# Kernel optimization log

Hardware: AMD Instinct MI355X
Metric: run time of the kernel (lower is better)

Reference implementation:

```python
import math
import jax, jax.numpy as jnp
import numpy as np

B, S, D = 32, 2048, 128

def setup_inputs() -> dict:
    key = jax.random.key(0)
    kq, kk, kv, km = jax.random.split(key, 4)
    q = jax.random.normal(kq, (B, S, D), dtype=jnp.float32)
    k = jax.random.normal(kk, (B, S, D), dtype=jnp.float32)
    v = jax.random.normal(kv, (B, S, D), dtype=jnp.float32)
    mask = jax.random.uniform(km, (B, S, S), dtype=jnp.float32)
    return {"q": q, "k": k, "v": v, "mask": mask}

def reference(q, k, v, mask):
    # scaled_product = (q @ k^T) / sqrt(d), then MULTIPLICATIVE mask, softmax, @ v
    scale = 1.0 / math.sqrt(k.shape[-1])
    scores = jnp.einsum("bqd,bkd->bqk", q, k) * scale  # [B, Sq, Sk]
    scores = scores * mask
    weights = jax.nn.softmax(scores, axis=-1)
    return jnp.einsum("bqk,bkd->bqd", weights, v)
```

## Files before the change

### kernel.cpp

```cpp
#include <hip/hip_runtime.h>
#include <math.h>

#define BATCH 32
#define SEQ   2048
#define DH    128
#define QT    64
#define KT    64
#define KSTR  136
#define VSTR  72
#define PSTR  72
#define SCALE 0.08838834764831845f

typedef _Float16 f16;
typedef _Float16 f16x4 __attribute__((ext_vector_type(4)));
typedef _Float16 f16x8 __attribute__((ext_vector_type(8)));
typedef float    f32x4 __attribute__((ext_vector_type(4)));

__global__ __launch_bounds__(256, 3)
void ScaledDotProductAttention_46720654246409_kernel(
    const float* __restrict__ q, const float* __restrict__ k,
    const float* __restrict__ v, const float* __restrict__ mask,
    float* __restrict__ out)
{
    __shared__ f16 ks[KT * KSTR];
    __shared__ f16 vs[DH * VSTR];
    __shared__ f16 ps[4 * 16 * PSTR];

    const int tid  = threadIdx.x;
    const int wv   = tid >> 6;
    const int lane = tid & 63;
    const int quad = lane >> 4;
    const int l16  = lane & 15;
    const int srow = tid >> 5;
    const int scol = tid & 31;

    const int bidx = blockIdx.x;
    const int b    = bidx >> 5;
    const int q0   = (bidx & 31) * QT;

    const size_t qkvBase = (size_t)b * SEQ * DH;
    const size_t mBase   = (size_t)b * SEQ * SEQ;

    #pragma unroll
    for (int p = 0; p < 8; ++p) {
        int r = p * 8 + srow;
        f32x4 x = *(const f32x4*)&q[qkvBase + (size_t)(q0 + r) * DH + scol * 4];
        f16x4 h = { (f16)x.x, (f16)x.y, (f16)x.z, (f16)x.w };
        *(f16x4*)&ks[r * KSTR + scol * 4] = h;
    }
    __syncthreads();

    f16x8 aq[4];
    #pragma unroll
    for (int dc = 0; dc < 4; ++dc)
        aq[dc] = *(const f16x8*)&ks[(wv * 16 + l16) * KSTR + dc * 32 + quad * 8];
    __syncthreads();

    float m_run[4] = { -INFINITY, -INFINITY, -INFINITY, -INFINITY };
    float l_run[4] = { 0.f, 0.f, 0.f, 0.f };
    f32x4 o[8];
    #pragma unroll
    for (int f = 0; f < 8; ++f) o[f] = (f32x4){0.f, 0.f, 0.f, 0.f};

    for (int kt = 0; kt < SEQ / KT; ++kt) {
        const int k0 = kt * KT;

        float mk[4][4];
        #pragma unroll
        for (int f = 0; f < 4; ++f)
            #pragma unroll
            for (int r = 0; r < 4; ++r)
                mk[f][r] = mask[mBase + (size_t)(q0 + wv*16 + quad*4 + r) * SEQ
                                + k0 + f*16 + l16];

        #pragma unroll
        for (int p = 0; p < 8; ++p) {
            int r = p * 8 + srow;
            f32x4 x = *(const f32x4*)&k[qkvBase + (size_t)(k0 + r) * DH + scol * 4];
            f16x4 h = { (f16)x.x, (f16)x.y, (f16)x.z, (f16)x.w };
            *(f16x4*)&ks[r * KSTR + scol * 4] = h;
        }
        #pragma unroll
        for (int p = 0; p < 8; ++p) {
            int j = p * 8 + srow;
            const float* vr = &v[qkvBase + (size_t)(k0 + j) * DH];
            #pragma unroll
            for (int i = 0; i < 4; ++i)
                vs[(scol + 32*i) * VSTR + j] = (f16)vr[scol + 32*i];
        }
        __syncthreads();

        f32x4 sc[4];
        #pragma unroll
        for (int f = 0; f < 4; ++f) {
            sc[f] = (f32x4){0.f, 0.f, 0.f, 0.f};
            #pragma unroll
            for (int dc = 0; dc < 4; ++dc) {
                f16x8 bk = *(const f16x8*)&ks[(f*16 + l16) * KSTR + dc*32 + quad*8];
                sc[f] = __builtin_amdgcn_mfma_f32_16x16x32_f16(aq[dc], bk, sc[f], 0, 0, 0);
            }
        }

        float pj[4][4];
        float alpha[4];
        #pragma unroll
        for (int r = 0; r < 4; ++r) {
            float sf[4];
            #pragma unroll
            for (int f = 0; f < 4; ++f) sf[f] = sc[f][r] * SCALE * mk[f][r];
            float mx = fmaxf(fmaxf(sf[0], sf[1]), fmaxf(sf[2], sf[3]));
            #pragma unroll
            for (int off = 1; off < 16; off <<= 1)
                mx = fmaxf(mx, __shfl_xor(mx, off, 16));
            float mn = fmaxf(m_run[r], mx);
            float al = __expf(m_run[r] - mn);
            float sum = 0.f;
            #pragma unroll
            for (int f = 0; f < 4; ++f) { pj[f][r] = __expf(sf[f] - mn); sum += pj[f][r]; }
            #pragma unroll
            for (int off = 1; off < 16; off <<= 1)
                sum += __shfl_xor(sum, off, 16);
            m_run[r] = mn;
            l_run[r] = l_run[r] * al + sum;
            alpha[r] = al;
        }

        #pragma unroll
        for (int f = 0; f < 4; ++f)
            #pragma unroll
            for (int r = 0; r < 4; ++r)
                ps[(wv*16 + quad*4 + r) * PSTR + f*16 + l16] = (f16)pj[f][r];
        asm volatile("s_waitcnt lgkmcnt(0)" ::: "memory");

        f16x8 ap0 = *(const f16x8*)&ps[(wv*16 + l16) * PSTR + quad*8];
        f16x8 ap1 = *(const f16x8*)&ps[(wv*16 + l16) * PSTR + 32 + quad*8];

        #pragma unroll
        for (int f = 0; f < 8; ++f) {
            #pragma unroll
            for (int r = 0; r < 4; ++r) o[f][r] *= alpha[r];
            f16x8 bv0 = *(const f16x8*)&vs[(f*16 + l16) * VSTR + quad*8];
            f16x8 bv1 = *(const f16x8*)&vs[(f*16 + l16) * VSTR + 32 + quad*8];
            o[f] = __builtin_amdgcn_mfma_f32_16x16x32_f16(ap0, bv0, o[f], 0, 0, 0);
            o[f] = __builtin_amdgcn_mfma_f32_16x16x32_f16(ap1, bv1, o[f], 0, 0, 0);
        }
        __syncthreads();
    }

    #pragma unroll
    for (int r = 0; r < 4; ++r) {
        float inv = 1.0f / l_run[r];
        #pragma unroll
        for (int f = 0; f < 8; ++f)
            out[qkvBase + (size_t)(q0 + wv*16 + quad*4 + r) * DH + f*16 + l16]
                = o[f][r] * inv;
    }
}

extern "C" void kernel_launch(void* const* d_in, const int* in_sizes, int n_in,
                              void* d_out, int out_size, void* d_ws, size_t ws_size,
                              hipStream_t stream) {
    const float* q    = (const float*)d_in[0];
    const float* k    = (const float*)d_in[1];
    const float* v    = (const float*)d_in[2];
    const float* mask = (const float*)d_in[3];
    float* out = (float*)d_out;

    dim3 grid(BATCH * (SEQ / QT));
    dim3 block(256);
    hipLaunchKernelGGL(ScaledDotProductAttention_46720654246409_kernel,
                       grid, block, 0, stream, q, k, v, mask, out);
}
```

Baseline: 884.5 us.

## Pre-convert K and transpose V to fp16 in workspace, load via global_load_lds

Adds two preprocessing kernels that convert K to fp16 and transpose V to fp16 in the workspace. The attention kernel then streams these tiles straight into XOR-swizzled LDS with direct global-to-LDS loads, and reads the mask as coalesced nontemporal vectors. It also transposes the score MFMA so each lane owns one query row, which reduces the softmax shuffle reductions. The aim is to remove the per-block fp32 conversion and strided V transpose that every query tile repeated for the same K/V. The cost is two extra launches, workspace traffic and a dependency on workspace size, with the old kernel kept as a fallback.

```diff
diff --git a/kernel.cpp b/kernel.cpp
--- a/kernel.cpp
+++ b/kernel.cpp
@@ -6,9 +6,6 @@
 #define DH    128
 #define QT    64
 #define KT    64
-#define KSTR  136
-#define VSTR  72
-#define PSTR  72
 #define SCALE 0.08838834764831845f
 
 typedef _Float16 f16;
@@ -16,15 +13,210 @@
 typedef _Float16 f16x8 __attribute__((ext_vector_type(8)));
 typedef float    f32x4 __attribute__((ext_vector_type(4)));
 
+__device__ __forceinline__ void gld16(const void* g, void* l) {
+    __builtin_amdgcn_global_load_lds(
+        (const __attribute__((address_space(1))) unsigned int*)g,
+        (__attribute__((address_space(3))) unsigned int*)l,
+        16, 0, 0);
+}
+
+__global__ __launch_bounds__(256)
+void cvt_k_kernel(const float* __restrict__ src, f16* __restrict__ dst) {
+    size_t i = ((size_t)blockIdx.x * 256 + threadIdx.x) * 8;
+    f32x4 a = *(const f32x4*)&src[i];
+    f32x4 c = *(const f32x4*)&src[i + 4];
+    f16x8 h = { (f16)a.x,(f16)a.y,(f16)a.z,(f16)a.w,(f16)c.x,(f16)c.y,(f16)c.z,(f16)c.w };
+    *(f16x8*)&dst[i] = h;
+}
+
+__global__ __launch_bounds__(256)
+void tr_v_kernel(const float* __restrict__ v, f16* __restrict__ vt) {
+    __shared__ f16 t[128 * 80];
+    const int tid  = threadIdx.x;
+    const int srow = tid >> 5, scol = tid & 31;
+    const int b  = blockIdx.x >> 5;
+    const int s0 = (blockIdx.x & 31) * 64;
+    const size_t base = (size_t)b * SEQ * DH;
+    #pragma unroll
+    for (int p = 0; p < 8; ++p) {
+        int j = p * 8 + srow;
+        const float* vr = &v[base + (size_t)(s0 + j) * DH];
+        #pragma unroll
+        for (int i = 0; i < 4; ++i)
+            t[(scol + 32 * i) * 80 + j] = (f16)vr[scol + 32 * i];
+    }
+    __syncthreads();
+    #pragma unroll
+    for (int p = 0; p < 4; ++p) {
+        int c = p * 256 + tid;
+        int d = c >> 3, col = (c & 7) * 8;
+        f16x8 h = *(const f16x8*)&t[d * 80 + col];
+        *(f16x8*)&vt[(size_t)b * DH * SEQ + (size_t)d * SEQ + s0 + col] = h;
+    }
+}
+
+__global__ __launch_bounds__(256, 4)
+void ScaledDotProductAttention_46720654246409_kernel(
+    const float* __restrict__ q, const f16* __restrict__ k16,
+    const f16* __restrict__ vt16, const float* __restrict__ mask,
+    float* __restrict__ out)
+{
+    __shared__ f16 ks[64 * 128];
+    __shared__ f16 vs[128 * 64];
+    __shared__ f16 ps[4 * 16 * 64];
+
+    const int tid  = threadIdx.x;
+    const int wv   = tid >> 6;
+    const int lane = tid & 63;
+    const int quad = lane >> 4;
+    const int l16  = lane & 15;
+    const int m3   = l16 & 7;
+    const int srow = tid >> 5;
+    const int scol = tid & 31;
+
+    const int bidx = blockIdx.x;
+    const int b    = bidx >> 5;
+    const int q0   = (bidx & 31) * QT;
+
+    const size_t qkvBase = (size_t)b * SEQ * DH;
+    const size_t mBase   = (size_t)b * SEQ * SEQ;
+
+    char* ksb = (char*)ks;
+    char* vsb = (char*)vs;
+    char* psb = (char*)ps + wv * 2048;
+
+    #pragma unroll
+    for (int p = 0; p < 8; ++p) {
+        int r = p * 8 + srow;
+        f32x4 x = *(const f32x4*)&q[qkvBase + (size_t)(q0 + r) * DH + scol * 4];
+        f16x4 h = { (f16)x.x, (f16)x.y, (f16)x.z, (f16)x.w };
+        *(f16x4*)(ksb + r * 256 + ((scol * 8) ^ ((r & 7) << 4))) = h;
+    }
+    __syncthreads();
+
+    f16x8 aq[4];
+    #pragma unroll
+    for (int dc = 0; dc < 4; ++dc)
+        aq[dc] = *(const f16x8*)(ksb + (wv * 16 + l16) * 256 + ((dc * 64 + quad * 16) ^ (m3 << 4)));
+    __syncthreads();
+
+    float m_run = -INFINITY, l_run = 0.f;
+    f32x4 o[8];
+    #pragma unroll
+    for (int f = 0; f < 8; ++f) o[f] = (f32x4){0.f, 0.f, 0.f, 0.f};
+
+    const f16* kbase = k16  + qkvBase;
+    const f16* vbase = vt16 + (size_t)b * DH * SEQ;
+
+    #pragma unroll 1
+    for (int kt = 0; kt < SEQ / KT; ++kt) {
+        const int k0 = kt * KT;
+
+        #pragma unroll
+        for (int i = 0; i < 4; ++i) {
+            int c   = wv * 4 + i;
+            int row = c * 4 + (lane >> 4);
+            gld16(kbase + (size_t)(k0 + row) * DH + 8 * ((lane & 15) ^ (row & 7)),
+                  ksb + c * 1024);
+        }
+        #pragma unroll
+        for (int i = 0; i < 4; ++i) {
+            int c   = wv * 4 + i;
+            int row = c * 8 + (lane >> 3);
+            gld16(vbase + (size_t)row * SEQ + k0 + 8 * ((lane & 7) ^ (row & 7)),
+                  vsb + c * 1024);
+        }
+
+        f32x4 mk[4];
+        const float* mrow = &mask[mBase + (size_t)(q0 + wv * 16 + l16) * SEQ + k0 + quad * 4];
+        #pragma unroll
+        for (int f = 0; f < 4; ++f)
+            mk[f] = __builtin_nontemporal_load((const f32x4*)(mrow + f * 16));
+
+        __syncthreads();
+
+        f32x4 sc[4];
+        #pragma unroll
+        for (int f = 0; f < 4; ++f) {
+            sc[f] = (f32x4){0.f, 0.f, 0.f, 0.f};
+            #pragma unroll
+            for (int dc = 0; dc < 4; ++dc) {
+                f16x8 kf = *(const f16x8*)(ksb + (f * 16 + l16) * 256 +
+                                           ((dc * 64 + quad * 16) ^ (m3 << 4)));
+                sc[f] = __builtin_amdgcn_mfma_f32_16x16x32_f16(kf, aq[dc], sc[f], 0, 0, 0);
+            }
+        }
+
+        float sf[4][4];
+        float mx = -INFINITY;
+        #pragma unroll
+        for (int f = 0; f < 4; ++f)
+            #pragma unroll
+            for (int r = 0; r < 4; ++r) {
+                sf[f][r] = sc[f][r] * SCALE * mk[f][r];
+                mx = fmaxf(mx, sf[f][r]);
+            }
+        mx = fmaxf(mx, __shfl_xor(mx, 16));
+        mx = fmaxf(mx, __shfl_xor(mx, 32));
+        float mn = fmaxf(m_run, mx);
+        float al = __expf(m_run - mn);
+        float sum = 0.f;
+        float pv[4][4];
+        #pragma unroll
+        for (int f = 0; f < 4; ++f)
+            #pragma unroll
+            for (int r = 0; r < 4; ++r) { pv[f][r] = __expf(sf[f][r] - mn); sum += pv[f][r]; }
+        sum += __shfl_xor(sum, 16);
+        sum += __shfl_xor(sum, 32);
+        m_run = mn;
+        l_run = l_run * al + sum;
+        float alpha[4];
+        #pragma unroll
+        for (int r = 0; r < 4; ++r) alpha[r] = __shfl(al, quad * 4 + r, 16);
+
+        #pragma unroll
+        for (int f = 0; f < 4; ++f) {
+            f16x4 pk = { (f16)pv[f][0], (f16)pv[f][1], (f16)pv[f][2], (f16)pv[f][3] };
+            *(f16x4*)(psb + l16 * 128 + ((f * 32 + quad * 8) ^ (m3 << 4))) = pk;
+        }
+        asm volatile("s_waitcnt lgkmcnt(0)" ::: "memory");
+
+        f16x8 ap0 = *(const f16x8*)(psb + l16 * 128 + ((quad * 16) ^ (m3 << 4)));
+        f16x8 ap1 = *(const f16x8*)(psb + l16 * 128 + ((64 + quad * 16) ^ (m3 << 4)));
+
+        #pragma unroll
+        for (int f = 0; f < 8; ++f) {
+            #pragma unroll
+            for (int r = 0; r < 4; ++r) o[f][r] *= alpha[r];
+            const char* vrow = vsb + (f * 16 + l16) * 128;
+            f16x8 bv0 = *(const f16x8*)(vrow + ((quad * 16) ^ (m3 << 4)));
+            f16x8 bv1 = *(const f16x8*)(vrow + ((64 + quad * 16) ^ (m3 << 4)));
+            o[f] = __builtin_amdgcn_mfma_f32_16x16x32_f16(ap0, bv0, o[f], 0, 0, 0);
+            o[f] = __builtin_amdgcn_mfma_f32_16x16x32_f16(ap1, bv1, o[f], 0, 0, 0);
+        }
+        __syncthreads();
+    }
+
+    float linv[4];
+    #pragma unroll
+    for (int r = 0; r < 4; ++r) linv[r] = 1.0f / __shfl(l_run, quad * 4 + r, 16);
+    #pragma unroll
+    for (int r = 0; r < 4; ++r)
+        #pragma unroll
+        for (int f = 0; f < 8; ++f)
+            __builtin_nontemporal_store(o[f][r] * linv[r],
+                &out[qkvBase + (size_t)(q0 + wv * 16 + quad * 4 + r) * DH + f * 16 + l16]);
+}
+
 __global__ __launch_bounds__(256, 3)
-void ScaledDotProductAttention_46720654246409_kernel(
+void attn_fallback_kernel(
     const float* __restrict__ q, const float* __restrict__ k,
     const float* __restrict__ v, const float* __restrict__ mask,
     float* __restrict__ out)
 {
-    __shared__ f16 ks[KT * KSTR];
-    __shared__ f16 vs[DH * VSTR];
-    __shared__ f16 ps[4 * 16 * PSTR];
+    __shared__ f16 ks[KT * 136];
+    __shared__ f16 vs[DH * 72];
+    __shared__ f16 ps[4 * 16 * 72];
 
     const int tid  = threadIdx.x;
     const int wv   = tid >> 6;
@@ -46,14 +238,14 @@
         int r = p * 8 + srow;
         f32x4 x = *(const f32x4*)&q[qkvBase + (size_t)(q0 + r) * DH + scol * 4];
         f16x4 h = { (f16)x.x, (f16)x.y, (f16)x.z, (f16)x.w };
-        *(f16x4*)&ks[r * KSTR + scol * 4] = h;
+        *(f16x4*)&ks[r * 136 + scol * 4] = h;
     }
     __syncthreads();
 
     f16x8 aq[4];
     #pragma unroll
     for (int dc = 0; dc < 4; ++dc)
-        aq[dc] = *(const f16x8*)&ks[(wv * 16 + l16) * KSTR + dc * 32 + quad * 8];
+        aq[dc] = *(const f16x8*)&ks[(wv * 16 + l16) * 136 + dc * 32 + quad * 8];
     __syncthreads();
 
     float m_run[4] = { -INFINITY, -INFINITY, -INFINITY, -INFINITY };
@@ -78,7 +270,7 @@
             int r = p * 8 + srow;
             f32x4 x = *(const f32x4*)&k[qkvBase + (size_t)(k0 + r) * DH + scol * 4];
             f16x4 h = { (f16)x.x, (f16)x.y, (f16)x.z, (f16)x.w };
-            *(f16x4*)&ks[r * KSTR + scol * 4] = h;
+            *(f16x4*)&ks[r * 136 + scol * 4] = h;
         }
         #pragma unroll
         for (int p = 0; p < 8; ++p) {
@@ -86,7 +278,7 @@
             const float* vr = &v[qkvBase + (size_t)(k0 + j) * DH];
             #pragma unroll
             for (int i = 0; i < 4; ++i)
-                vs[(scol + 32*i) * VSTR + j] = (f16)vr[scol + 32*i];
+                vs[(scol + 32*i) * 72 + j] = (f16)vr[scol + 32*i];
         }
         __syncthreads();
 
@@ -96,7 +288,7 @@
             sc[f] = (f32x4){0.f, 0.f, 0.f, 0.f};
             #pragma unroll
             for (int dc = 0; dc < 4; ++dc) {
-                f16x8 bk = *(const f16x8*)&ks[(f*16 + l16) * KSTR + dc*32 + quad*8];
+                f16x8 bk = *(const f16x8*)&ks[(f*16 + l16) * 136 + dc*32 + quad*8];
                 sc[f] = __builtin_amdgcn_mfma_f32_16x16x32_f16(aq[dc], bk, sc[f], 0, 0, 0);
             }
         }
@@ -129,18 +321,18 @@
         for (int f = 0; f < 4; ++f)
             #pragma unroll
             for (int r = 0; r < 4; ++r)
-                ps[(wv*16 + quad*4 + r) * PSTR + f*16 + l16] = (f16)pj[f][r];
+                ps[(wv*16 + quad*4 + r) * 72 + f*16 + l16] = (f16)pj[f][r];
         asm volatile("s_waitcnt lgkmcnt(0)" ::: "memory");
 
-        f16x8 ap0 = *(const f16x8*)&ps[(wv*16 + l16) * PSTR + quad*8];
-        f16x8 ap1 = *(const f16x8*)&ps[(wv*16 + l16) * PSTR + 32 + quad*8];
+        f16x8 ap0 = *(const f16x8*)&ps[(wv*16 + l16) * 72 + quad*8];
+        f16x8 ap1 = *(const f16x8*)&ps[(wv*16 + l16) * 72 + 32 + quad*8];
 
         #pragma unroll
         for (int f = 0; f < 8; ++f) {
             #pragma unroll
             for (int r = 0; r < 4; ++r) o[f][r] *= alpha[r];
-            f16x8 bv0 = *(const f16x8*)&vs[(f*16 + l16) * VSTR + quad*8];
-            f16x8 bv1 = *(const f16x8*)&vs[(f*16 + l16) * VSTR + 32 + quad*8];
+            f16x8 bv0 = *(const f16x8*)&vs[(f*16 + l16) * 72 + quad*8];
+            f16x8 bv1 = *(const f16x8*)&vs[(f*16 + l16) * 72 + 32 + quad*8];
             o[f] = __builtin_amdgcn_mfma_f32_16x16x32_f16(ap0, bv0, o[f], 0, 0, 0);
             o[f] = __builtin_amdgcn_mfma_f32_16x16x32_f16(ap1, bv1, o[f], 0, 0, 0);
         }
@@ -166,8 +358,20 @@
     const float* mask = (const float*)d_in[3];
     float* out = (float*)d_out;
 
-    dim3 grid(BATCH * (SEQ / QT));
-    dim3 block(256);
-    hipLaunchKernelGGL(ScaledDotProductAttention_46720654246409_kernel,
-                       grid, block, 0, stream, q, k, v, mask, out);
-}
+    const size_t elems = (size_t)BATCH * SEQ * DH;
+    if (d_ws && ws_size >= 2 * elems * sizeof(f16)) {
+        f16* k16  = (f16*)d_ws;
+        f16* vt16 = k16 + elems;
+        hipLaunchKernelGGL(cvt_k_kernel, dim3((unsigned)(elems / 2048)), dim3(256), 0, stream,
+                           k, k16);
+        hipLaunchKernelGGL(tr_v_kernel, dim3(BATCH * (SEQ / 64)), dim3(256), 0, stream,
+                           v, vt16);
+        hipLaunchKernelGGL(ScaledDotProductAttention_46720654246409_kernel,
+                           dim3(BATCH * (SEQ / QT)), dim3(256), 0, stream,
+                           q, k16, vt16, mask, out);
+    } else {
+        hipLaunchKernelGGL(attn_fallback_kernel,
+                           dim3(BATCH * (SEQ / QT)), dim3(256), 0, stream,
+                           q, k, v, mask, out);
+    }
+}
```

Result: faster. 812.0 us (-8.2%).
